# Kernel optimization log

Measured on AMD Instinct MI355X. Metric: run time of the kernel, lower is better.

## Reference

```python
import jax, jax.numpy as jnp
import numpy as np

E = 8          # n_experts
TOP_K = 2      # n_active_experts


def setup_inputs() -> dict:
    key = jax.random.key(0)
    ks = jax.random.split(key, 9)
    B, S, D, H = 4, 2048, 2048, 1408
    w = 0.02  # weight scale for numerical stability
    return {
        "x": jax.random.normal(ks[0], (B, S, D), dtype=jnp.float32),
        "gate_w": jax.random.normal(ks[1], (E, D), dtype=jnp.float32) * w,
        "expert_bias": jnp.zeros((E,), dtype=jnp.float32),
        "Wg": jax.random.normal(ks[2], (E, H, D), dtype=jnp.float32) * w,
        "Wu": jax.random.normal(ks[3], (E, H, D), dtype=jnp.float32) * w,
        "Wd": jax.random.normal(ks[4], (E, D, H), dtype=jnp.float32) * w,
        "Ws_g": jax.random.normal(ks[5], (H, D), dtype=jnp.float32) * w,
        "Ws_u": jax.random.normal(ks[6], (H, D), dtype=jnp.float32) * w,
        "Ws_d": jax.random.normal(ks[7], (D, H), dtype=jnp.float32) * w,
    }


def _swiglu(x, wg, wu, wd):
    # torch Linear layout: y = x @ W.T
    return (jax.nn.silu(x @ wg.T) * (x @ wu.T)) @ wd.T


def reference(x, gate_w, expert_bias, Wg, Wu, Wd, Ws_g, Ws_u, Ws_d):
    B, S, D = x.shape
    flat = x.reshape(-1, D)                      # [N, D]
    N = flat.shape[0]

    logits = flat @ gate_w.T                     # [N, E]
    probs = jax.nn.softmax(logits, axis=-1)
    biased = logits + expert_bias
    _, top_idx = jax.lax.top_k(biased, TOP_K)    # [N, K] (bias used only for selection)
    top_w = jnp.take_along_axis(probs, top_idx, axis=-1)
    top_w = top_w / jnp.sum(top_w, axis=-1, keepdims=True)

    # dense per-token combine weights: cw[n, e] = sum_k top_w[n,k] * (top_idx[n,k]==e)
    rows = jnp.arange(N)[:, None]
    cw = jnp.zeros((N, E), dtype=flat.dtype).at[rows, top_idx].add(top_w)

    out = jnp.zeros_like(flat)
    for e in range(E):  # fixed small expert count; equivalent to gather/scatter dispatch
        out = out + cw[:, e:e + 1] * _swiglu(flat, Wg[e], Wu[e], Wd[e])

    out = out + _swiglu(flat, Ws_g, Ws_u, Ws_d)  # shared expert
    return out.reshape(B, S, D)
```

## Files before the change

kernel.cpp:

```cpp
#include <hip/hip_runtime.h>
#include <hip/hip_bf16.h>

#define N_TOK 8192
#define DDIM  2048
#define HDIM  1408
#define ROWS_R 16384
#define ROWS_T 24576
#define MAXTILES 104
#define BM 256
#define BN 128
#define BK 64

typedef unsigned short u16;
typedef unsigned int   u32;
typedef __bf16 bf16x8 __attribute__((ext_vector_type(8)));
typedef float  f32x4  __attribute__((ext_vector_type(4)));

__device__ __forceinline__ u16 f2bf(float f) {
  union { float f; u32 u; } v; v.f = f;
  u32 u = v.u;
  return (u16)((u + 0x7fffu + ((u >> 16) & 1u)) >> 16);
}
__device__ __forceinline__ float bf2f(u16 b) {
  union { u32 u; float f; } v; v.u = ((u32)b) << 16; return v.f;
}

typedef __attribute__((address_space(1))) void gvoid;
typedef __attribute__((address_space(3))) void lvoid;
__device__ __forceinline__ void gload16(const void* g, void* l) {
  __builtin_amdgcn_global_load_lds((gvoid*)g, (lvoid*)l, 16, 0, 0);
}

#define BAR __builtin_amdgcn_s_barrier()
#define SP1 __builtin_amdgcn_s_setprio(1)
#define SP0 __builtin_amdgcn_s_setprio(0)
#define LGK0 do { asm volatile("s_waitcnt lgkmcnt(0)" ::: "memory"); \
                  __builtin_amdgcn_sched_barrier(0); } while (0)
#define VMCNT(n) asm volatile("s_waitcnt vmcnt(" #n ")" ::: "memory")

#define READ_AF(base, mb, dst) { \
  _Pragma("unroll") for (int m_ = 0; m_ < 2; ++m_) { \
    int r_ = wr * 64 + ((mb) + m_) * 16 + l15; \
    _Pragma("unroll") for (int kk_ = 0; kk_ < 2; ++kk_) { \
      int cch_ = kk_ * 4 + lhi; \
      (dst)[m_ * 2 + kk_] = *(const bf16x8*)((const char*)(base) + r_ * 128 + ((cch_ ^ (r_ & 7)) * 16)); } } }

#define READ_BF(base, dst) { \
  _Pragma("unroll") for (int n_ = 0; n_ < 4; ++n_) { \
    int r_ = wc * 64 + n_ * 16 + l15; \
    _Pragma("unroll") for (int kk_ = 0; kk_ < 2; ++kk_) { \
      int cch_ = kk_ * 4 + lhi; \
      (dst)[n_ * 2 + kk_] = *(const bf16x8*)((const char*)(base) + r_ * 128 + ((cch_ ^ (r_ & 7)) * 16)); } } }

#define MFMAQ(AF, BB, ACC, MB) { \
  _Pragma("unroll") for (int m_ = 0; m_ < 2; ++m_) \
  _Pragma("unroll") for (int n_ = 0; n_ < 4; ++n_) \
  _Pragma("unroll") for (int kk_ = 0; kk_ < 2; ++kk_) \
    (ACC)[(MB) + m_][n_] = __builtin_amdgcn_mfma_f32_16x16x32_bf16((AF)[m_ * 2 + kk_], (BB)[n_ * 2 + kk_], (ACC)[(MB) + m_][n_], 0, 0, 0); }

__global__ void k_gate(const float* __restrict__ x, const float* __restrict__ gw,
                       const float* __restrict__ bias, int* __restrict__ tok_idx,
                       float* __restrict__ wts, int* __restrict__ counts,
                       u16* __restrict__ xb) {
  int lane = threadIdx.x & 63;
  int n = blockIdx.x * 4 + (threadIdx.x >> 6);
  const float* xr = x + (size_t)n * DDIM;
  u16* xbr = xb + (size_t)n * DDIM;
  float acc[8];
#pragma unroll
  for (int e = 0; e < 8; ++e) acc[e] = 0.f;
#pragma unroll 2
  for (int j0 = 0; j0 < DDIM; j0 += 256) {
    float4 xv = *(const float4*)(xr + j0 + lane * 4);
    u32 p0 = (u32)f2bf(xv.x) | ((u32)f2bf(xv.y) << 16);
    u32 p1 = (u32)f2bf(xv.z) | ((u32)f2bf(xv.w) << 16);
    *(uint2*)(xbr + j0 + lane * 4) = make_uint2(p0, p1);
#pragma unroll
    for (int e = 0; e < 8; ++e) {
      float4 gv = *(const float4*)(gw + e * DDIM + j0 + lane * 4);
      acc[e] += xv.x * gv.x + xv.y * gv.y + xv.z * gv.z + xv.w * gv.w;
    }
  }
#pragma unroll
  for (int e = 0; e < 8; ++e) {
#pragma unroll
    for (int off = 32; off > 0; off >>= 1) acc[e] += __shfl_xor(acc[e], off);
  }
  if (lane == 0) {
    float m = acc[0];
    for (int e = 1; e < 8; ++e) m = fmaxf(m, acc[e]);
    float p[8];
    for (int e = 0; e < 8; ++e) p[e] = expf(acc[e] - m);
    float b0[8];
    for (int e = 0; e < 8; ++e) b0[e] = acc[e] + bias[e];
    int i0 = 0;
    for (int e = 1; e < 8; ++e) if (b0[e] > b0[i0]) i0 = e;
    int i1 = (i0 == 0) ? 1 : 0;
    for (int e = 0; e < 8; ++e) if (e != i0 && b0[e] > b0[i1]) i1 = e;
    float w0 = p[i0], w1 = p[i1], inv = 1.f / (w0 + w1);
    tok_idx[2 * n] = i0; tok_idx[2 * n + 1] = i1;
    wts[2 * n] = w0 * inv; wts[2 * n + 1] = w1 * inv;
    atomicAdd(&counts[i0], 1); atomicAdd(&counts[i1], 1);
  }
}

__global__ void k_scan(const int* __restrict__ counts, int* __restrict__ offsets,
                       int* __restrict__ cursors, int* __restrict__ ntiles,
                       int4* __restrict__ tiles) {
  if (threadIdx.x != 0 || blockIdx.x != 0) return;
  int off = 0, idx = 0;
  for (int e = 0; e < 8; ++e) {
    offsets[e] = off; cursors[e] = 0;
    int T = counts[e];
    for (int r = 0; r < T; r += BM) {
      int nr = T - r; if (nr > BM) nr = BM;
      tiles[idx++] = make_int4(e, off + r, nr, 0);
    }
    off += T;
  }
  offsets[8] = off;
  for (int r = 0; r < N_TOK; r += BM)
    tiles[idx++] = make_int4(8, ROWS_R + r, BM, 0);
  *ntiles = idx;
}

__global__ void k_build(const int* __restrict__ tok_idx, const int* __restrict__ offsets,
                        int* __restrict__ cursors, int* __restrict__ token_ids,
                        int* __restrict__ pos) {
  int n = blockIdx.x * blockDim.x + threadIdx.x;
  if (n >= N_TOK) return;
#pragma unroll
  for (int s = 0; s < 2; ++s) {
    int e = tok_idx[2 * n + s];
    int p = offsets[e] + atomicAdd(&cursors[e], 1);
    token_ids[p] = n;
    pos[2 * n + s] = p;
  }
  token_ids[ROWS_R + n] = n;
}

__global__ void k_conv(const float* __restrict__ src, u16* __restrict__ dst, long n8) {
  long stride = (long)gridDim.x * blockDim.x;
  for (long i = (long)blockIdx.x * blockDim.x + threadIdx.x; i < n8; i += stride) {
    const float4* s = (const float4*)(src) + i * 2;
    float4 a = s[0], b = s[1];
    u32 p0 = (u32)f2bf(a.x) | ((u32)f2bf(a.y) << 16);
    u32 p1 = (u32)f2bf(a.z) | ((u32)f2bf(a.w) << 16);
    u32 p2 = (u32)f2bf(b.x) | ((u32)f2bf(b.y) << 16);
    u32 p3 = (u32)f2bf(b.z) | ((u32)f2bf(b.w) << 16);
    ((uint4*)dst)[i] = make_uint4(p0, p1, p2, p3);
  }
}

__global__ __launch_bounds__(512, 2) void k_gemm1(
    const u16* __restrict__ xb, const u16* __restrict__ wgb,
    const int* __restrict__ token_ids, const int* __restrict__ ntiles,
    const int4* __restrict__ tiles, u16* __restrict__ h) {
  __shared__ u16 As[2][BM * BK];
  __shared__ u16 Bgs[2][BN * BK];
  __shared__ u16 Bus[2][BN * BK];

  int ntl = *ntiles;
  int nwg = (HDIM / BN) * ntl;
  int bid = blockIdx.x;
  if (bid >= nwg) return;
  int q8 = nwg >> 3, r8 = nwg & 7;
  int xcd = bid & 7, pp = bid >> 3;
  int lid = (xcd < r8 ? xcd * (q8 + 1) : r8 * (q8 + 1) + (xcd - r8) * q8) + pp;
  int bx = lid / ntl, tile = lid - bx * ntl;

  int4 tl = tiles[tile];
  int set = tl.x, grow = tl.y, nrows = tl.z;

  int t = threadIdx.x;
  int wid = t >> 6, lane = t & 63;
  int wr = wid >> 1, wc = wid & 1;
  int l15 = lane & 15, lhi = lane >> 4;

  const u16* aptr[4];
#pragma unroll
  for (int i = 0; i < 4; ++i) {
    int chunk = i * 512 + t;
    int r = chunk >> 3, cc = chunk & 7;
    int c = cc ^ (r & 7);
    int rr = r < nrows ? r : nrows - 1;
    int tok = token_ids[grow + rr];
    aptr[i] = xb + (size_t)tok * DDIM + c * 8;
  }
  const u16* gptr[2];
#pragma unroll
  for (int i = 0; i < 2; ++i) {
    int chunk = i * 512 + t;
    int r = chunk >> 3, cc = chunk & 7;
    int c = cc ^ (r & 7);
    gptr[i] = wgb + (size_t)set * (HDIM * DDIM) + (size_t)(bx * BN + r) * DDIM + c * 8;
  }
  const size_t WUOFF = (size_t)9 * HDIM * DDIM;

#define G1_A0(b, k0) { gload16(aptr[0] + (k0), (char*)As[b] + (size_t)t * 16); \
                       gload16(aptr[1] + (k0), (char*)As[b] + (size_t)(512 + t) * 16); }
#define G1_A1(b, k0) { gload16(aptr[2] + (k0), (char*)As[b] + (size_t)(1024 + t) * 16); \
                       gload16(aptr[3] + (k0), (char*)As[b] + (size_t)(1536 + t) * 16); }
#define G1_BG(b, k0) { gload16(gptr[0] + (k0), (char*)Bgs[b] + (size_t)t * 16); \
                       gload16(gptr[1] + (k0), (char*)Bgs[b] + (size_t)(512 + t) * 16); }
#define G1_BU(b, k0) { gload16(gptr[0] + WUOFF + (k0), (char*)Bus[b] + (size_t)t * 16); \
                       gload16(gptr[1] + WUOFF + (k0), (char*)Bus[b] + (size_t)(512 + t) * 16); }

  f32x4 accg[4][4], accu[4][4];
  f32x4 z = {0.f, 0.f, 0.f, 0.f};
#pragma unroll
  for (int m = 0; m < 4; ++m)
#pragma unroll
    for (int n = 0; n < 4; ++n) { accg[m][n] = z; accu[m][n] = z; }

  const int NK = DDIM / BK;

  VMCNT(0);
  G1_A0(0, 0); G1_A1(0, 0); G1_BG(0, 0); G1_BU(0, 0);
  VMCNT(2); BAR;

  for (int kt = 0; kt < NK - 1; ++kt) {
    int cur = kt & 1, nxt = cur ^ 1;
    int k1 = (kt + 1) * BK;
    bf16x8 a01[4], a23[4], bb[8];
    READ_AF(As[cur], 0, a01);
    READ_BF(Bgs[cur], bb);
    G1_A0(nxt, k1);
    BAR; LGK0;
    SP1; MFMAQ(a01, bb, accg, 0); SP0;
    BAR;
    READ_AF(As[cur], 2, a23);
    G1_A1(nxt, k1);
    BAR; LGK0;
    SP1; MFMAQ(a23, bb, accg, 2); SP0;
    VMCNT(4); BAR;
    READ_BF(Bus[cur], bb);
    G1_BG(nxt, k1);
    BAR; LGK0;
    SP1; MFMAQ(a01, bb, accu, 0); SP0;
    BAR;
    G1_BU(nxt, k1);
    BAR;
    SP1; MFMAQ(a23, bb, accu, 2); SP0;
    VMCNT(2); BAR;
  }
  {
    int cur = (NK - 1) & 1;
    VMCNT(0); BAR;
    bf16x8 a01[4], a23[4], bg8[8], bu8[8];
    READ_AF(As[cur], 0, a01);
    READ_AF(As[cur], 2, a23);
    READ_BF(Bgs[cur], bg8);
    READ_BF(Bus[cur], bu8);
    LGK0;
    MFMAQ(a01, bg8, accg, 0); MFMAQ(a23, bg8, accg, 2);
    MFMAQ(a01, bu8, accu, 0); MFMAQ(a23, bu8, accu, 2);
  }

#pragma unroll
  for (int m = 0; m < 4; ++m) {
#pragma unroll
    for (int n = 0; n < 4; ++n) {
      int col = bx * BN + wc * 64 + n * 16 + l15;
#pragma unroll
      for (int qq = 0; qq < 4; ++qq) {
        int rl = wr * 64 + m * 16 + lhi * 4 + qq;
        if (rl < nrows) {
          float g = accg[m][n][qq], u = accu[m][n][qq];
          float hv = g / (1.f + expf(-g)) * u;
          h[(size_t)(grow + rl) * HDIM + col] = f2bf(hv);
        }
      }
    }
  }
#undef G1_A0
#undef G1_A1
#undef G1_BG
#undef G1_BU
}

__global__ __launch_bounds__(512, 2) void k_gemm2(
    const u16* __restrict__ h, const u16* __restrict__ wdb,
    const int* __restrict__ ntiles, const int4* __restrict__ tiles,
    u16* __restrict__ y) {
  __shared__ u16 As2[3][BM * BK];
  __shared__ u16 Bs2[3][BN * BK];

  int ntl = *ntiles;
  int nwg = (DDIM / BN) * ntl;
  int bid = blockIdx.x;
  if (bid >= nwg) return;
  int q8 = nwg >> 3, r8 = nwg & 7;
  int xcd = bid & 7, pp = bid >> 3;
  int lid = (xcd < r8 ? xcd * (q8 + 1) : r8 * (q8 + 1) + (xcd - r8) * q8) + pp;
  int bx = lid / ntl, tile = lid - bx * ntl;

  int4 tl = tiles[tile];
  int set = tl.x, grow = tl.y, nrows = tl.z;

  int t = threadIdx.x;
  int wid = t >> 6, lane = t & 63;
  int wr = wid >> 1, wc = wid & 1;
  int l15 = lane & 15, lhi = lane >> 4;

  const u16* aptr[4];
#pragma unroll
  for (int i = 0; i < 4; ++i) {
    int chunk = i * 512 + t;
    int r = chunk >> 3, cc = chunk & 7;
    int c = cc ^ (r & 7);
    aptr[i] = h + (size_t)(grow + r) * HDIM + c * 8;
  }
  const u16* bptr[2];
#pragma unroll
  for (int i = 0; i < 2; ++i) {
    int chunk = i * 512 + t;
    int r = chunk >> 3, cc = chunk & 7;
    int c = cc ^ (r & 7);
    bptr[i] = wdb + (size_t)set * (DDIM * HDIM) + (size_t)(bx * BN + r) * HDIM + c * 8;
  }

#define G2_A(b, k0) { gload16(aptr[0] + (k0), (char*)As2[b] + (size_t)t * 16); \
                      gload16(aptr[1] + (k0), (char*)As2[b] + (size_t)(512 + t) * 16); \
                      gload16(aptr[2] + (k0), (char*)As2[b] + (size_t)(1024 + t) * 16); \
                      gload16(aptr[3] + (k0), (char*)As2[b] + (size_t)(1536 + t) * 16); }
#define G2_B(b, k0) { gload16(bptr[0] + (k0), (char*)Bs2[b] + (size_t)t * 16); \
                      gload16(bptr[1] + (k0), (char*)Bs2[b] + (size_t)(512 + t) * 16); }

  f32x4 acc[4][4];
  f32x4 z = {0.f, 0.f, 0.f, 0.f};
#pragma unroll
  for (int m = 0; m < 4; ++m)
#pragma unroll
    for (int n = 0; n < 4; ++n) acc[m][n] = z;

  const int NK2 = HDIM / BK;

  VMCNT(0);
  G2_A(0, 0); G2_B(0, 0);
  G2_A(1, BK); G2_B(1, BK);
  VMCNT(6); BAR;

  for (int kt = 0; kt < NK2 - 2; ++kt) {
    int cur = kt % 3, nx2 = (kt + 2) % 3;
    int k2 = (kt + 2) * BK;
    bf16x8 a01[4], a23[4], bb[8];
    READ_AF(As2[cur], 0, a01);
    READ_BF(Bs2[cur], bb);
    G2_A(nx2, k2);
    BAR; LGK0;
    SP1; MFMAQ(a01, bb, acc, 0); SP0;
    BAR;
    READ_AF(As2[cur], 2, a23);
    G2_B(nx2, k2);
    BAR; LGK0;
    SP1; MFMAQ(a23, bb, acc, 2); SP0;
    VMCNT(6); BAR;
  }
  VMCNT(0); BAR;
  for (int kt = NK2 - 2; kt < NK2; ++kt) {
    int cur = kt % 3;
    bf16x8 a01[4], a23[4], bb[8];
    READ_AF(As2[cur], 0, a01);
    READ_AF(As2[cur], 2, a23);
    READ_BF(Bs2[cur], bb);
    LGK0;
    MFMAQ(a01, bb, acc, 0); MFMAQ(a23, bb, acc, 2);
  }

#pragma unroll
  for (int m = 0; m < 4; ++m) {
#pragma unroll
    for (int n = 0; n < 4; ++n) {
      int col = bx * BN + wc * 64 + n * 16 + l15;
#pragma unroll
      for (int qq = 0; qq < 4; ++qq) {
        int rl = wr * 64 + m * 16 + lhi * 4 + qq;
        if (rl < nrows)
          y[(size_t)(grow + rl) * DDIM + col] = f2bf(acc[m][n][qq]);
      }
    }
  }
#undef G2_A
#undef G2_B
}

__global__ void k_comb(const u16* __restrict__ y, const int* __restrict__ pos,
                       const float* __restrict__ wts, float* __restrict__ out) {
  int n = blockIdx.x;
  int c8 = threadIdx.x;
  int p0 = pos[2 * n], p1 = pos[2 * n + 1];
  float w0 = wts[2 * n], w1 = wts[2 * n + 1];
  uint4 a = ((const uint4*)(y + (size_t)p0 * DDIM))[c8];
  uint4 b = ((const uint4*)(y + (size_t)p1 * DDIM))[c8];
  uint4 c = ((const uint4*)(y + (size_t)(ROWS_R + n) * DDIM))[c8];
  float* o = out + (size_t)n * DDIM + c8 * 8;
#pragma unroll
  for (int j = 0; j < 4; ++j) {
    u32 ua = ((const u32*)&a)[j], ub = ((const u32*)&b)[j], uc = ((const u32*)&c)[j];
    o[2 * j]     = w0 * bf2f((u16)(ua & 0xffff)) + w1 * bf2f((u16)(ub & 0xffff)) + bf2f((u16)(uc & 0xffff));
    o[2 * j + 1] = w0 * bf2f((u16)(ua >> 16))    + w1 * bf2f((u16)(ub >> 16))    + bf2f((u16)(uc >> 16));
  }
}

extern "C" void kernel_launch(void* const* d_in, const int* in_sizes, int n_in,
                              void* d_out, int out_size, void* d_ws, size_t ws_size,
                              hipStream_t stream) {
  const float* x    = (const float*)d_in[0];
  const float* gw   = (const float*)d_in[1];
  const float* bias = (const float*)d_in[2];
  const float* Wg   = (const float*)d_in[3];
  const float* Wu   = (const float*)d_in[4];
  const float* Wd   = (const float*)d_in[5];
  const float* Wsg  = (const float*)d_in[6];
  const float* Wsu  = (const float*)d_in[7];
  const float* Wsd  = (const float*)d_in[8];
  float* out = (float*)d_out;

  char* ws = (char*)d_ws;
  size_t off = 0;
  auto alloc = [&](size_t bytes) -> void* {
    void* p = ws + off;
    off += (bytes + 255) & ~(size_t)255;
    return p;
  };
  u16* xb  = (u16*)alloc((size_t)N_TOK * DDIM * 2);
  u16* wgb = (u16*)alloc((size_t)9 * HDIM * DDIM * 2);
  u16* wub = (u16*)alloc((size_t)9 * HDIM * DDIM * 2);
  u16* wdb = (u16*)alloc((size_t)9 * DDIM * HDIM * 2);
  u16* h   = (u16*)alloc((size_t)ROWS_T * HDIM * 2);
  u16* y   = (u16*)alloc((size_t)ROWS_T * DDIM * 2);
  int*   token_ids = (int*)alloc(ROWS_T * 4);
  int*   tok_idx   = (int*)alloc(N_TOK * 2 * 4);
  int*   pos       = (int*)alloc(N_TOK * 2 * 4);
  float* wts       = (float*)alloc(N_TOK * 2 * 4);
  int*   counts  = (int*)alloc(8 * 4);
  int*   offsets = (int*)alloc(9 * 4);
  int*   cursors = (int*)alloc(8 * 4);
  int*   ntiles  = (int*)alloc(4);
  int4*  tiles   = (int4*)alloc(MAXTILES * 16);

  hipMemsetAsync(counts, 0, 8 * 4, stream);
  k_gate<<<N_TOK / 4, 256, 0, stream>>>(x, gw, bias, tok_idx, wts, counts, xb);
  k_scan<<<1, 64, 0, stream>>>(counts, offsets, cursors, ntiles, tiles);
  k_build<<<(N_TOK + 255) / 256, 256, 0, stream>>>(tok_idx, offsets, cursors, token_ids, pos);

  k_conv<<<4096, 256, 0, stream>>>(Wg, wgb, (long)8 * HDIM * DDIM / 8);
  k_conv<<<512, 256, 0, stream>>>(Wsg, wgb + (size_t)8 * HDIM * DDIM, (long)HDIM * DDIM / 8);
  k_conv<<<4096, 256, 0, stream>>>(Wu, wub, (long)8 * HDIM * DDIM / 8);
  k_conv<<<512, 256, 0, stream>>>(Wsu, wub + (size_t)8 * HDIM * DDIM, (long)HDIM * DDIM / 8);
  k_conv<<<4096, 256, 0, stream>>>(Wd, wdb, (long)8 * DDIM * HDIM / 8);
  k_conv<<<512, 256, 0, stream>>>(Wsd, wdb + (size_t)8 * DDIM * HDIM, (long)DDIM * HDIM / 8);

  k_gemm1<<<(HDIM / BN) * MAXTILES, 512, 0, stream>>>(xb, wgb, token_ids, ntiles, tiles, h);
  k_gemm2<<<(DDIM / BN) * MAXTILES, 512, 0, stream>>>(h, wdb, ntiles, tiles, y);
  k_comb<<<N_TOK, 256, 0, stream>>>(y, pos, wts, out);
}
```

Before: 935.8 us.

## Merge weight conversions, reorder gemm1 prefetch stages, remap warp row ownership

Replaces the six weight-conversion launches with one grid-stride kernel that handles all the weight arrays, removing launch overhead and tail effects. In gemm1, the gate B tile is now prefetched first and the vmcnt waits are adjusted, so the next-tile loads issue in a different order relative to the MFMA phases. The A-fragment row mapping and the epilogue row index are changed so each warp row-group owns two interleaved 32-row slabs instead of one contiguous 64-row slab, which shifts the LDS access pattern. The reordered waits could expose load latency or race if the counts do not match the loads still in flight.

```diff
diff --git a/kernel.cpp b/kernel.cpp
--- a/kernel.cpp
+++ b/kernel.cpp
@@ -40,7 +40,7 @@
 
 #define READ_AF(base, mb, dst) { \
   _Pragma("unroll") for (int m_ = 0; m_ < 2; ++m_) { \
-    int r_ = wr * 64 + ((mb) + m_) * 16 + l15; \
+    int r_ = ((mb) >> 1) * 128 + wr * 32 + m_ * 16 + l15; \
     _Pragma("unroll") for (int kk_ = 0; kk_ < 2; ++kk_) { \
       int cch_ = kk_ * 4 + lhi; \
       (dst)[m_ * 2 + kk_] = *(const bf16x8*)((const char*)(base) + r_ * 128 + ((cch_ ^ (r_ & 7)) * 16)); } } }
@@ -139,16 +139,27 @@
   token_ids[ROWS_R + n] = n;
 }
 
-__global__ void k_conv(const float* __restrict__ src, u16* __restrict__ dst, long n8) {
+__global__ void k_convall(const float* __restrict__ Wg, const float* __restrict__ Wsg,
+                          const float* __restrict__ Wu, const float* __restrict__ Wsu,
+                          const float* __restrict__ Wd, const float* __restrict__ Wsd,
+                          u16* __restrict__ wgb, u16* __restrict__ wub, u16* __restrict__ wdb) {
+  const long PER = (long)9 * HDIM * DDIM / 8;
+  const long BIG = (long)8 * HDIM * DDIM / 8;
+  const long TOT = 3 * PER;
   long stride = (long)gridDim.x * blockDim.x;
-  for (long i = (long)blockIdx.x * blockDim.x + threadIdx.x; i < n8; i += stride) {
-    const float4* s = (const float4*)(src) + i * 2;
-    float4 a = s[0], b = s[1];
+  for (long i = (long)blockIdx.x * blockDim.x + threadIdx.x; i < TOT; i += stride) {
+    int g = (int)(i / PER);
+    long r = i - (long)g * PER;
+    const float* src; u16* dst;
+    if (g == 0)      { dst = wgb; src = (r < BIG) ? Wg + r * 8 : Wsg + (r - BIG) * 8; }
+    else if (g == 1) { dst = wub; src = (r < BIG) ? Wu + r * 8 : Wsu + (r - BIG) * 8; }
+    else             { dst = wdb; src = (r < BIG) ? Wd + r * 8 : Wsd + (r - BIG) * 8; }
+    float4 a = ((const float4*)src)[0], b = ((const float4*)src)[1];
     u32 p0 = (u32)f2bf(a.x) | ((u32)f2bf(a.y) << 16);
     u32 p1 = (u32)f2bf(a.z) | ((u32)f2bf(a.w) << 16);
     u32 p2 = (u32)f2bf(b.x) | ((u32)f2bf(b.y) << 16);
     u32 p3 = (u32)f2bf(b.z) | ((u32)f2bf(b.w) << 16);
-    ((uint4*)dst)[i] = make_uint4(p0, p1, p2, p3);
+    ((uint4*)dst)[r] = make_uint4(p0, p1, p2, p3);
   }
 }
 
@@ -216,8 +227,8 @@
   const int NK = DDIM / BK;
 
   VMCNT(0);
-  G1_A0(0, 0); G1_A1(0, 0); G1_BG(0, 0); G1_BU(0, 0);
-  VMCNT(2); BAR;
+  G1_BG(0, 0); G1_A0(0, 0); G1_A1(0, 0); G1_BU(0, 0);
+  VMCNT(4); BAR;
 
   for (int kt = 0; kt < NK - 1; ++kt) {
     int cur = kt & 1, nxt = cur ^ 1;
@@ -225,24 +236,24 @@
     bf16x8 a01[4], a23[4], bb[8];
     READ_AF(As[cur], 0, a01);
     READ_BF(Bgs[cur], bb);
-    G1_A0(nxt, k1);
+    G1_BG(nxt, k1);
     BAR; LGK0;
     SP1; MFMAQ(a01, bb, accg, 0); SP0;
-    BAR;
+    VMCNT(4); BAR;
     READ_AF(As[cur], 2, a23);
-    G1_A1(nxt, k1);
+    G1_A0(nxt, k1);
     BAR; LGK0;
     SP1; MFMAQ(a23, bb, accg, 2); SP0;
     VMCNT(4); BAR;
     READ_BF(Bus[cur], bb);
-    G1_BG(nxt, k1);
+    G1_A1(nxt, k1);
     BAR; LGK0;
     SP1; MFMAQ(a01, bb, accu, 0); SP0;
     BAR;
     G1_BU(nxt, k1);
     BAR;
     SP1; MFMAQ(a23, bb, accu, 2); SP0;
-    VMCNT(2); BAR;
+    VMCNT(4); BAR;
   }
   {
     int cur = (NK - 1) & 1;
@@ -264,7 +275,7 @@
       int col = bx * BN + wc * 64 + n * 16 + l15;
 #pragma unroll
       for (int qq = 0; qq < 4; ++qq) {
-        int rl = wr * 64 + m * 16 + lhi * 4 + qq;
+        int rl = (m >> 1) * 128 + wr * 32 + (m & 1) * 16 + lhi * 4 + qq;
         if (rl < nrows) {
           float g = accg[m][n][qq], u = accu[m][n][qq];
           float hv = g / (1.f + expf(-g)) * u;
@@ -375,7 +386,7 @@
       int col = bx * BN + wc * 64 + n * 16 + l15;
 #pragma unroll
       for (int qq = 0; qq < 4; ++qq) {
-        int rl = wr * 64 + m * 16 + lhi * 4 + qq;
+        int rl = (m >> 1) * 128 + wr * 32 + (m & 1) * 16 + lhi * 4 + qq;
         if (rl < nrows)
           y[(size_t)(grow + rl) * DDIM + col] = f2bf(acc[m][n][qq]);
       }
@@ -445,12 +456,7 @@
   k_scan<<<1, 64, 0, stream>>>(counts, offsets, cursors, ntiles, tiles);
   k_build<<<(N_TOK + 255) / 256, 256, 0, stream>>>(tok_idx, offsets, cursors, token_ids, pos);
 
-  k_conv<<<4096, 256, 0, stream>>>(Wg, wgb, (long)8 * HDIM * DDIM / 8);
-  k_conv<<<512, 256, 0, stream>>>(Wsg, wgb + (size_t)8 * HDIM * DDIM, (long)HDIM * DDIM / 8);
-  k_conv<<<4096, 256, 0, stream>>>(Wu, wub, (long)8 * HDIM * DDIM / 8);
-  k_conv<<<512, 256, 0, stream>>>(Wsu, wub + (size_t)8 * HDIM * DDIM, (long)HDIM * DDIM / 8);
-  k_conv<<<4096, 256, 0, stream>>>(Wd, wdb, (long)8 * DDIM * HDIM / 8);
-  k_conv<<<512, 256, 0, stream>>>(Wsd, wdb + (size_t)8 * DDIM * HDIM, (long)DDIM * HDIM / 8);
+  k_convall<<<4096, 256, 0, stream>>>(Wg, Wsg, Wu, Wsu, Wd, Wsd, wgb, wub, wdb);
 
   k_gemm1<<<(HDIM / BN) * MAXTILES, 512, 0, stream>>>(xb, wgb, token_ids, ntiles, tiles, h);
   k_gemm2<<<(DDIM / BN) * MAXTILES, 512, 0, stream>>>(h, wdb, ntiles, tiles, y);
```

After: 963.5 us. 1.03x slower.
